# Performance work log

Hardware: AMD Instinct MI355X
Metric: run time of the kernel (lower is better)

## Reference

```python
import jax, jax.numpy as jnp
import numpy as np

B, C, H, W = 4, 192, 256, 256
WS = 8           # window_size
NH = 6           # num_heads
RS = 0.1         # residual_scale
RED = C // 16    # channel-attention reduced channels
HID = 4 * C      # ffn hidden
EPS = 1e-5


def _rel_pos_index(ws):
    coords = np.stack(np.meshgrid(np.arange(ws), np.arange(ws), indexing='ij'))  # [2,ws,ws]
    cf = coords.reshape(2, -1)
    rel = cf[:, :, None] - cf[:, None, :]            # [2,N,N]
    rel = rel.transpose(1, 2, 0).copy()
    rel[:, :, 0] += ws - 1
    rel[:, :, 1] += ws - 1
    rel[:, :, 0] *= 2 * ws - 1
    return jnp.asarray(rel.sum(-1))                  # [N,N] int

RPI = _rel_pos_index(WS)


def setup_inputs() -> dict:
    key = jax.random.key(0)
    ks = jax.random.split(key, 16)
    s = 0.02
    return {
        'x': jax.random.normal(ks[0], (B, C, H, W), jnp.float32),
        'n1_w': jnp.ones((C,), jnp.float32), 'n1_b': jnp.zeros((C,), jnp.float32),
        'n2_w': jnp.ones((C,), jnp.float32), 'n2_b': jnp.zeros((C,), jnp.float32),
        'n3_w': jnp.ones((C,), jnp.float32), 'n3_b': jnp.zeros((C,), jnp.float32),
        'ca_w1': jax.random.normal(ks[1], (RED, C), jnp.float32) * s,
        'ca_w2': jax.random.normal(ks[2], (C, RED), jnp.float32) * s,
        'qkv_w': jax.random.normal(ks[3], (3 * C, C), jnp.float32) * s,
        'proj_w': jax.random.normal(ks[4], (C, C), jnp.float32) * s,
        'proj_b': jnp.zeros((C,), jnp.float32),
        'rpb': jax.random.normal(ks[5], ((2 * WS - 1) ** 2, NH), jnp.float32) * s,
        'ffn_w1': jax.random.normal(ks[6], (HID, C), jnp.float32) * s,
        'ffn_b1': jnp.zeros((HID,), jnp.float32),
        'ffn_w2': jax.random.normal(ks[7], (C, HID), jnp.float32) * s,
        'ffn_b2': jnp.zeros((C,), jnp.float32),
    }


def _ln(x, w, b):
    m = x.mean(-1, keepdims=True)
    v = x.var(-1, keepdims=True)
    return (x - m) * jax.lax.rsqrt(v + EPS) * w + b


def reference(x, n1_w, n1_b, n2_w, n2_b, n3_w, n3_b, ca_w1, ca_w2,
              qkv_w, proj_w, proj_b, rpb, ffn_w1, ffn_b1, ffn_w2, ffn_b2):
    # --- channel attention branch ---
    res = x                                             # [B,C,H,W]
    xc = _ln(x.transpose(0, 2, 3, 1), n1_w, n1_b)       # [B,H,W,C]
    xc = xc.transpose(0, 3, 1, 2)                       # [B,C,H,W]
    y = xc.mean(axis=(2, 3))                            # [B,C] global avg pool
    y = jax.nn.relu(y @ ca_w1.T) @ ca_w2.T              # [B,C]
    y = jax.nn.sigmoid(y)[:, :, None, None]
    x = xc * y * RS + res

    # --- window attention branch ---
    res = x
    xw = _ln(x.transpose(0, 2, 3, 1), n2_w, n2_b)       # [B,H,W,C]
    nH, nW, N = H // WS, W // WS, WS * WS
    xw = xw.reshape(B, nH, WS, nW, WS, C).transpose(0, 1, 3, 2, 4, 5)
    xw = xw.reshape(B * nH * nW, N, C)                  # [Bn,N,C]

    d = C // NH
    qkv = (xw @ qkv_w.T).reshape(-1, N, 3, NH, d).transpose(2, 0, 3, 1, 4)
    q, k, v = qkv[0], qkv[1], qkv[2]                    # [Bn,NH,N,d]
    q = q * (d ** -0.5)
    attn = jnp.einsum('bhnd,bhmd->bhnm', q, k)          # [Bn,NH,N,N]
    bias = rpb[RPI.reshape(-1)].reshape(N, N, NH).transpose(2, 0, 1)
    attn = jax.nn.softmax(attn + bias[None], axis=-1)
    o = jnp.einsum('bhnm,bhmd->bhnd', attn, v)
    o = o.transpose(0, 2, 1, 3).reshape(-1, N, C)
    o = o @ proj_w.T + proj_b

    o = _ln(o, n3_w, n3_b)
    h = jax.nn.gelu(o @ ffn_w1.T + ffn_b1, approximate=False)
    o = o + (h @ ffn_w2.T + ffn_b2) * RS

    o = o.reshape(B, nH, nW, WS, WS, C).transpose(0, 1, 3, 2, 4, 5)
    o = o.reshape(B, H, W, C).transpose(0, 3, 1, 2)     # [B,C,H,W]
    return o * RS + res
```

## Files before the change

### kernel.cpp

```cpp
#include <hip/hip_runtime.h>
#include <math.h>

#define CC    192
#define WWD   256
#define HWSZ  65536
#define BB    4
#define NHD   6
#define HIDDEN 768
#define RSC   0.1f
#define EPSV  1e-5f

typedef short s8v __attribute__((ext_vector_type(8)));
typedef float f4v __attribute__((ext_vector_type(4)));
#define MFMA16(a,b,c) __builtin_amdgcn_mfma_f32_16x16x32_bf16(a,b,c,0,0,0)

__device__ __forceinline__ float b2f(unsigned short h){
  return __uint_as_float(((unsigned int)h) << 16);
}
__device__ __forceinline__ unsigned short f2b(float f){
  unsigned int u = __float_as_uint(f);
  u += 0x7FFFu + ((u >> 16) & 1u);
  return (unsigned short)(u >> 16);
}
__device__ __forceinline__ float wredsum(float v){
  #pragma unroll
  for (int off = 32; off > 0; off >>= 1) v += __shfl_xor(v, off, 64);
  return v;
}

__global__ __launch_bounds__(256) void k0_all(
    const float* __restrict__ s0, const float* __restrict__ s1,
    const float* __restrict__ s2, const float* __restrict__ s3,
    unsigned short* __restrict__ d0, unsigned short* __restrict__ d1,
    unsigned short* __restrict__ d2, unsigned short* __restrict__ d3)
{
  int i = blockIdx.x * 256 + threadIdx.x;
  const float* s; unsigned short* d; int off;
  if (i < 27648)      { s = s0; d = d0; off = 0; }
  else if (i < 36864) { s = s1; d = d1; off = 27648; }
  else if (i < 73728) { s = s2; d = d2; off = 36864; }
  else                { s = s3; d = d3; off = 73728; }
  int j = i - off;
  float4 v = ((const float4*)s)[j];
  ((ushort4*)d)[j] = make_ushort4(f2b(v.x), f2b(v.y), f2b(v.z), f2b(v.w));
}

__global__ __launch_bounds__(256) void k1a_stats(
    const float* __restrict__ x, float2* __restrict__ mr)
{
  __shared__ float red[2048];
  const int pg = threadIdx.x & 63;
  const int sl = threadIdx.x >> 6;
  const int G  = blockIdx.x * 64 + pg;
  const int b  = G >> 14;
  const float* xp = x + (size_t)(b * CC) * HWSZ + ((size_t)(G & 16383) << 2);

  float sx=0.f, sy=0.f, sz=0.f, sw=0.f;
  float qx=0.f, qy=0.f, qz=0.f, qw=0.f;
  #pragma unroll 4
  for (int i = 0; i < 48; ++i){
    float4 v = *(const float4*)(xp + (size_t)(sl * 48 + i) * HWSZ);
    sx += v.x; qx += v.x * v.x;
    sy += v.y; qy += v.y * v.y;
    sz += v.z; qz += v.z * v.z;
    sw += v.w; qw += v.w * v.w;
  }
  float* rp = red + threadIdx.x * 8;
  rp[0]=sx; rp[1]=sy; rp[2]=sz; rp[3]=sw;
  rp[4]=qx; rp[5]=qy; rp[6]=qz; rp[7]=qw;
  __syncthreads();
  if (sl == 0){
    #pragma unroll
    for (int s = 1; s < 4; ++s){
      const float* o = red + (s * 64 + pg) * 8;
      sx += o[0]; sy += o[1]; sz += o[2]; sw += o[3];
      qx += o[4]; qy += o[5]; qz += o[6]; qw += o[7];
    }
    const float inv = 1.f / CC;
    float m0 = sx*inv, m1 = sy*inv, m2 = sz*inv, m3 = sw*inv;
    float4* mrv = (float4*)mr;
    mrv[G*2]   = make_float4(m0, rsqrtf(qx*inv - m0*m0 + EPSV),
                             m1, rsqrtf(qy*inv - m1*m1 + EPSV));
    mrv[G*2+1] = make_float4(m2, rsqrtf(qz*inv - m2*m2 + EPSV),
                             m3, rsqrtf(qw*inv - m3*m3 + EPSV));
  }
}

__global__ __launch_bounds__(256) void k1b_pool(
    const float* __restrict__ x, const float4* __restrict__ mrv,
    const float* __restrict__ n1w, const float* __restrict__ n1b,
    float* __restrict__ pool)
{
  int phys = blockIdx.x;
  int b = phys & 3, c = phys >> 2;
  const float4* xp = (const float4*)(x + (size_t)(b * CC + c) * HWSZ);
  const float4* mp = mrv + (size_t)b * 32768;
  float acc = 0.f;
  for (int g = threadIdx.x; g < 16384; g += 256){
    float4 v   = xp[g];
    float4 m01 = mp[2*g], m23 = mp[2*g+1];
    acc += (v.x - m01.x) * m01.y + (v.y - m01.z) * m01.w
         + (v.z - m23.x) * m23.y + (v.w - m23.z) * m23.w;
  }
  acc = wredsum(acc);
  __shared__ float r4[4];
  if ((threadIdx.x & 63) == 0) r4[threadIdx.x >> 6] = acc;
  __syncthreads();
  if (threadIdx.x == 0)
    pool[b * CC + c] = n1w[c] * (r4[0] + r4[1] + r4[2] + r4[3])
                       + 65536.f * n1b[c];
}

__global__ __launch_bounds__(256) void k2_camlp(
    const float* __restrict__ pool, const float* __restrict__ w1,
    const float* __restrict__ w2, float* __restrict__ sig)
{
  __shared__ float t[BB * 12];
  int tid = threadIdx.x;
  if (tid < BB * 12){
    int b = tid / 12, r = tid % 12;
    float a = 0.f;
    for (int c = 0; c < CC; ++c) a += pool[b * CC + c] * w1[r * CC + c];
    a *= (1.f / 65536.f);
    t[tid] = fmaxf(a, 0.f);
  }
  __syncthreads();
  for (int i = tid; i < BB * CC; i += 256){
    int b = i / CC, c = i - b * CC;
    float z = 0.f;
    #pragma unroll
    for (int r = 0; r < 12; ++r) z += t[b * 12 + r] * w2[c * 12 + r];
    sig[i] = 1.f / (1.f + __expf(-z));
  }
}

__global__ void __launch_bounds__(256)
__attribute__((amdgpu_waves_per_eu(3, 3)))
k4_win(
    const float* __restrict__ x, const float2* __restrict__ mr,
    const float* __restrict__ sig,
    const float* __restrict__ n1w, const float* __restrict__ n1b,
    const float* __restrict__ n2w, const float* __restrict__ n2b,
    const float* __restrict__ n3w, const float* __restrict__ n3b,
    const unsigned short* __restrict__ qw,
    const unsigned short* __restrict__ pw,
    const float* __restrict__ projb,
    const float* __restrict__ rpb,
    const unsigned short* __restrict__ f1w,
    const float* __restrict__ fb1,
    const unsigned short* __restrict__ f2w,
    const float* __restrict__ fb2,
    float* __restrict__ out)
{
  __shared__ __align__(16) unsigned short lds[26624];
  unsigned short* Xs  = lds;
  unsigned short* Qs  = lds + 12800;
  unsigned short* Ks  = lds + 17408;
  unsigned short* VsT = lds + 22016;
  unsigned short* Hs  = lds + 12800;
  unsigned short* Ov  = lds + 12800;

  const int tid  = threadIdx.x;
  const int lane = tid & 63;
  const int wv   = tid >> 6;
  const int l15  = lane & 15;
  const int q    = lane >> 4;

  int phys = blockIdx.x;
  int blk  = ((phys & 7) << 9) | (phys >> 3);
  int b   = blk >> 10;
  int wh  = (blk >> 5) & 31;
  int ww  = blk & 31;
  size_t base = (size_t)(b * CC) * HWSZ + (size_t)(wh * 8) * WWD + ww * 8;
  int pbase = (b << 16) | ((wh * 8) << 8) | (ww * 8);

  float4 x1v[12];
  #pragma unroll
  for (int kk = 0; kk < 12; ++kk){
    int idx = kk * 256 + tid;
    int c   = idx >> 4;
    int t   = idx & 15;
    int row = t >> 1, col0 = (t & 1) * 4;
    float4 xv = *(const float4*)(x + base + (size_t)c * HWSZ + row * WWD + col0);
    int px = pbase + row * 256 + col0;
    float4 mra = *(const float4*)(mr + px);
    float4 mrb = *(const float4*)(mr + px + 2);
    float w  = n1w[c], bv = n1b[c];
    float sv = sig[b * CC + c] * RSC;
    int n0 = row * 8 + col0;
    float4 o;
    o.x = ((xv.x - mra.x) * mra.y * w + bv) * sv + xv.x;
    o.y = ((xv.y - mra.z) * mra.w * w + bv) * sv + xv.y;
    o.z = ((xv.z - mrb.x) * mrb.y * w + bv) * sv + xv.z;
    o.w = ((xv.w - mrb.z) * mrb.w * w + bv) * sv + xv.w;
    x1v[kk] = o;
    Xs[(n0    ) * 200 + c] = f2b(o.x);
    Xs[(n0 + 1) * 200 + c] = f2b(o.y);
    Xs[(n0 + 2) * 200 + c] = f2b(o.z);
    Xs[(n0 + 3) * 200 + c] = f2b(o.w);
  }
  __syncthreads();

  {
    float wa = n2w[lane], wb = n2w[lane + 64], wc = n2w[lane + 128];
    float ba = n2b[lane], bb3 = n2b[lane + 64], bc = n2b[lane + 128];
    for (int n = wv; n < 64; n += 4){
      float v0 = b2f(Xs[n * 200 + lane]);
      float v1 = b2f(Xs[n * 200 + lane + 64]);
      float v2 = b2f(Xs[n * 200 + lane + 128]);
      float s  = wredsum(v0 + v1 + v2);
      float ss = wredsum(v0 * v0 + v1 * v1 + v2 * v2);
      float mean = s * (1.f / CC);
      float rstd = rsqrtf(ss * (1.f / CC) - mean * mean + EPSV);
      Xs[n * 200 + lane]       = f2b((v0 - mean) * rstd * wa + ba);
      Xs[n * 200 + lane + 64]  = f2b((v1 - mean) * rstd * wb + bb3);
      Xs[n * 200 + lane + 128] = f2b((v2 - mean) * rstd * wc + bc);
    }
  }
  __syncthreads();

  float oreg[12][4];
  for (int pr = 0; pr < 3; ++pr){
    for (int t3 = 0; t3 < 3; ++t3){
      int t = wv * 3 + t3;
      int sel = t >> 2;
      int s = t & 3;
      const unsigned short* wrow = qw + (size_t)(sel * 192 + pr * 64 + s * 16 + l15) * 192;
      s8v Bf[6];
      #pragma unroll
      for (int k = 0; k < 6; ++k) Bf[k] = *(const s8v*)(wrow + k * 32 + q * 8);
      #pragma unroll
      for (int mt = 0; mt < 4; ++mt){
        f4v acc = {0.f, 0.f, 0.f, 0.f};
        #pragma unroll
        for (int k = 0; k < 6; ++k){
          s8v Af = *(const s8v*)&Xs[(mt * 16 + l15) * 200 + k * 32 + q * 8];
          acc = MFMA16(Af, Bf[k], acc);
        }
        int row0 = mt * 16 + q * 4;
        if (sel == 0){
          #pragma unroll
          for (int r = 0; r < 4; ++r)
            Qs[(row0 + r) * 72 + s * 16 + l15] = f2b(acc[r] * 0.17677669529663689f);
        } else if (sel == 1){
          #pragma unroll
          for (int r = 0; r < 4; ++r)
            Ks[(row0 + r) * 72 + s * 16 + l15] = f2b(acc[r]);
        } else {
          #pragma unroll
          for (int r = 0; r < 4; ++r)
            VsT[(s * 16 + l15) * 72 + row0 + r] = f2b(acc[r]);
        }
      }
    }
    __syncthreads();

    float sc[2][4][4];
    {
      const s8v Aq0 = *(const s8v*)&Qs[(wv * 16 + l15) * 72 + q * 8];
      const s8v Aq1 = *(const s8v*)&Qs[(wv * 16 + l15) * 72 + 32 + q * 8];
      #pragma unroll
      for (int nt = 0; nt < 4; ++nt){
        s8v Bk0 = *(const s8v*)&Ks[(nt * 16 + l15) * 72 + q * 8];
        s8v Bk1 = *(const s8v*)&Ks[(nt * 16 + l15) * 72 + 32 + q * 8];
        f4v a0 = {0.f, 0.f, 0.f, 0.f};
        f4v a1 = {0.f, 0.f, 0.f, 0.f};
        a0 = MFMA16(Aq0, Bk0, a0);
        a1 = MFMA16(Aq1, Bk1, a1);
        #pragma unroll
        for (int r = 0; r < 4; ++r){ sc[0][nt][r] = a0[r]; sc[1][nt][r] = a1[r]; }
      }
    }
    #pragma unroll
    for (int hh = 0; hh < 2; ++hh){
      int h = pr * 2 + hh;
      #pragma unroll
      for (int r = 0; r < 4; ++r){
        int rt = wv * 16 + q * 4 + r;
        int i1 = rt >> 3, j1 = rt & 7;
        float mx = -1e30f;
        #pragma unroll
        for (int nt = 0; nt < 4; ++nt){
          int ct = nt * 16 + l15;
          int i2 = ct >> 3, j2 = ct & 7;
          sc[hh][nt][r] += rpb[((i1 - i2 + 7) * 15 + (j1 - j2 + 7)) * NHD + h];
          mx = fmaxf(mx, sc[hh][nt][r]);
        }
        #pragma unroll
        for (int m = 1; m <= 8; m <<= 1) mx = fmaxf(mx, __shfl_xor(mx, m, 64));
        float sm = 0.f;
        #pragma unroll
        for (int nt = 0; nt < 4; ++nt){
          sc[hh][nt][r] = __expf(sc[hh][nt][r] - mx);
          sm += sc[hh][nt][r];
        }
        #pragma unroll
        for (int m = 1; m <= 8; m <<= 1) sm += __shfl_xor(sm, m, 64);
        float invs = 1.f / sm;
        #pragma unroll
        for (int nt = 0; nt < 4; ++nt) sc[hh][nt][r] *= invs;
      }
    }
    #pragma unroll
    for (int hh = 0; hh < 2; ++hh){
      #pragma unroll
      for (int r = 0; r < 4; ++r)
        #pragma unroll
        for (int nt = 0; nt < 4; ++nt)
          Qs[(wv * 16 + q * 4 + r) * 72 + nt * 16 + l15] = f2b(sc[hh][nt][r]);
      #pragma unroll
      for (int vt = 0; vt < 2; ++vt){
        f4v acc = {0.f, 0.f, 0.f, 0.f};
        #pragma unroll
        for (int kst = 0; kst < 2; ++kst){
          s8v Ap = *(const s8v*)&Qs[(wv * 16 + l15) * 72 + kst * 32 + q * 8];
          s8v Bv = *(const s8v*)&VsT[(hh * 32 + vt * 16 + l15) * 72 + kst * 32 + q * 8];
          acc = MFMA16(Ap, Bv, acc);
        }
        int oi = (pr * 2 + hh) * 2 + vt;
        #pragma unroll
        for (int r = 0; r < 4; ++r) oreg[oi][r] = acc[r];
      }
    }
    __syncthreads();
  }

  #pragma unroll
  for (int oi = 0; oi < 12; ++oi){
    int h2 = oi >> 1, vt = oi & 1;
    int col = h2 * 32 + vt * 16 + l15;
    int row0 = wv * 16 + q * 4;
    #pragma unroll
    for (int r = 0; r < 4; ++r)
      Xs[(row0 + r) * 200 + col] = f2b(oreg[oi][r]);
  }
  __syncthreads();

  f4v pa[3][4];
  for (int j = 0; j < 3; ++j){
    int col = wv * 48 + j * 16 + l15;
    const unsigned short* wrow = pw + (size_t)col * 192;
    s8v Bf[6];
    #pragma unroll
    for (int k = 0; k < 6; ++k) Bf[k] = *(const s8v*)(wrow + k * 32 + q * 8);
    float bv = projb[col];
    #pragma unroll
    for (int mt = 0; mt < 4; ++mt){
      f4v acc = {bv, bv, bv, bv};
      #pragma unroll
      for (int k = 0; k < 6; ++k){
        s8v Af = *(const s8v*)&Xs[(mt * 16 + l15) * 200 + k * 32 + q * 8];
        acc = MFMA16(Af, Bf[k], acc);
      }
      pa[j][mt] = acc;
    }
  }
  __syncthreads();
  #pragma unroll
  for (int j = 0; j < 3; ++j)
    for (int mt = 0; mt < 4; ++mt)
      #pragma unroll
      for (int r = 0; r < 4; ++r)
        Xs[(mt * 16 + q * 4 + r) * 200 + wv * 48 + j * 16 + l15] = f2b(pa[j][mt][r]);
  __syncthreads();

  {
    float wa = n3w[lane], wb = n3w[lane + 64], wc = n3w[lane + 128];
    float ba = n3b[lane], bb3 = n3b[lane + 64], bc = n3b[lane + 128];
    for (int n = wv; n < 64; n += 4){
      float v0 = b2f(Xs[n * 200 + lane]);
      float v1 = b2f(Xs[n * 200 + lane + 64]);
      float v2 = b2f(Xs[n * 200 + lane + 128]);
      float s  = wredsum(v0 + v1 + v2);
      float ss = wredsum(v0 * v0 + v1 * v1 + v2 * v2);
      float mean = s * (1.f / CC);
      float rstd = rsqrtf(ss * (1.f / CC) - mean * mean + EPSV);
      Xs[n * 200 + lane]       = f2b((v0 - mean) * rstd * wa + ba);
      Xs[n * 200 + lane + 64]  = f2b((v1 - mean) * rstd * wb + bb3);
      Xs[n * 200 + lane + 128] = f2b((v2 - mean) * rstd * wc + bc);
    }
  }
  __syncthreads();

  f4v facc[3][4];
  #pragma unroll
  for (int j = 0; j < 3; ++j){
    float bv = fb2[wv * 48 + j * 16 + l15];
    #pragma unroll
    for (int mt = 0; mt < 4; ++mt) facc[j][mt] = (f4v){bv, bv, bv, bv};
  }
  for (int hc = 0; hc < 6; ++hc){
    for (int j = 0; j < 2; ++j){
      int hcol = hc * 128 + wv * 32 + j * 16 + l15;
      const unsigned short* wrow = f1w + (size_t)hcol * 192;
      s8v Bf[6];
      #pragma unroll
      for (int k = 0; k < 6; ++k) Bf[k] = *(const s8v*)(wrow + k * 32 + q * 8);
      float bv = fb1[hcol];
      #pragma unroll
      for (int mt = 0; mt < 4; ++mt){
        f4v acc = {bv, bv, bv, bv};
        #pragma unroll
        for (int k = 0; k < 6; ++k){
          s8v Af = *(const s8v*)&Xs[(mt * 16 + l15) * 200 + k * 32 + q * 8];
          acc = MFMA16(Af, Bf[k], acc);
        }
        #pragma unroll
        for (int r = 0; r < 4; ++r){
          float g = acc[r];
          g = 0.5f * g * (1.f + erff(g * 0.70710678118654752f));
          Hs[(mt * 16 + q * 4 + r) * 136 + wv * 32 + j * 16 + l15] = f2b(g);
        }
      }
    }
    __syncthreads();
    for (int j = 0; j < 3; ++j){
      int col = wv * 48 + j * 16 + l15;
      const unsigned short* wrow = f2w + (size_t)col * HIDDEN + hc * 128;
      s8v Bf[4];
      #pragma unroll
      for (int kst = 0; kst < 4; ++kst) Bf[kst] = *(const s8v*)(wrow + kst * 32 + q * 8);
      #pragma unroll
      for (int mt = 0; mt < 4; ++mt){
        f4v acc = facc[j][mt];
        #pragma unroll
        for (int kst = 0; kst < 4; ++kst){
          s8v Af = *(const s8v*)&Hs[(mt * 16 + l15) * 136 + kst * 32 + q * 8];
          acc = MFMA16(Af, Bf[kst], acc);
        }
        facc[j][mt] = acc;
      }
    }
    __syncthreads();
  }

  #pragma unroll
  for (int j = 0; j < 3; ++j)
    for (int mt = 0; mt < 4; ++mt)
      #pragma unroll
      for (int r = 0; r < 4; ++r){
        int row = mt * 16 + q * 4 + r;
        int col = wv * 48 + j * 16 + l15;
        float lv = b2f(Xs[row * 200 + col]);
        Ov[row * 196 + col] = f2b(lv + facc[j][mt][r] * RSC);
      }
  __syncthreads();

  #pragma unroll
  for (int kk = 0; kk < 12; ++kk){
    int idx = kk * 256 + tid;
    int c   = idx >> 4;
    int t   = idx & 15;
    int row = t >> 1, col0 = (t & 1) * 4;
    size_t gi = base + (size_t)c * HWSZ + row * WWD + col0;
    int n0 = row * 8 + col0;
    float4 o;
    o.x = b2f(Ov[(n0    ) * 196 + c]) * RSC + x1v[kk].x;
    o.y = b2f(Ov[(n0 + 1) * 196 + c]) * RSC + x1v[kk].y;
    o.z = b2f(Ov[(n0 + 2) * 196 + c]) * RSC + x1v[kk].z;
    o.w = b2f(Ov[(n0 + 3) * 196 + c]) * RSC + x1v[kk].w;
    *(float4*)(out + gi) = o;
  }
}

extern "C" void kernel_launch(void* const* d_in, const int* in_sizes, int n_in,
                              void* d_out, int out_size, void* d_ws, size_t ws_size,
                              hipStream_t stream)
{
  const float* x    = (const float*)d_in[0];
  const float* n1w  = (const float*)d_in[1];
  const float* n1b  = (const float*)d_in[2];
  const float* n2w  = (const float*)d_in[3];
  const float* n2b  = (const float*)d_in[4];
  const float* n3w  = (const float*)d_in[5];
  const float* n3b  = (const float*)d_in[6];
  const float* caw1 = (const float*)d_in[7];
  const float* caw2 = (const float*)d_in[8];
  const float* qkvw = (const float*)d_in[9];
  const float* projw= (const float*)d_in[10];
  const float* projb= (const float*)d_in[11];
  const float* rpb  = (const float*)d_in[12];
  const float* fw1  = (const float*)d_in[13];
  const float* fb1  = (const float*)d_in[14];
  const float* fw2  = (const float*)d_in[15];
  const float* fb2  = (const float*)d_in[16];
  float* out = (float*)d_out;

  float*  pool = (float*)d_ws;
  float*  sig  = pool + 768;
  float2* mr   = (float2*)(sig + 768);
  unsigned short* qw  = (unsigned short*)((char*)d_ws + 6144 + 2097152);
  unsigned short* pwb = qw  + 110592;
  unsigned short* f1b = pwb + 36864;
  unsigned short* f2b_ = f1b + 147456;

  k0_all<<<dim3(432), dim3(256), 0, stream>>>(qkvw, projw, fw1, fw2,
                                              qw, pwb, f1b, f2b_);
  k1a_stats<<<dim3(1024), dim3(256), 0, stream>>>(x, mr);
  k1b_pool <<<dim3(768),  dim3(256), 0, stream>>>(x, (const float4*)mr,
                                                  n1w, n1b, pool);
  k2_camlp <<<dim3(1),    dim3(256), 0, stream>>>(pool, caw1, caw2, sig);
  k4_win   <<<dim3(4096), dim3(256), 0, stream>>>(x, mr, sig, n1w, n1b,
                n2w, n2b, n3w, n3b, qw, pwb, projb, rpb, f1b, fb1, f2b_, fb2, out);
}
```

Baseline: 1.172 ms.

## Pack residual in bf16 registers, tanh GELU, 16-lane layernorm, nontemporal stores

The saved residual x1 is now kept as packed bf16 pairs (24 registers instead of 48 floats), which cuts register pressure. The exact erf GELU is replaced with a tanh approximation built on __expf. The two LayerNorms use 16-lane row groups with fewer shuffles and preload the weights into registers. Output stores are now nontemporal. The bf16 residual and the tanh GELU both reduce accuracy, since the residual x1 is added at bf16 precision.

```diff
diff --git a/kernel.cpp b/kernel.cpp
--- a/kernel.cpp
+++ b/kernel.cpp
@@ -26,6 +26,12 @@
   #pragma unroll
   for (int off = 32; off > 0; off >>= 1) v += __shfl_xor(v, off, 64);
   return v;
+}
+__device__ __forceinline__ float gelu(float g){
+  float u = g * (0.7978845608028654f + 0.0356774081363001f * g * g);
+  float e = __expf(-2.f * fabsf(u));
+  float t = __builtin_copysignf((1.f - e) / (1.f + e), u);
+  return 0.5f * g * (1.f + t);
 }
 
 __global__ __launch_bounds__(256) void k0_all(
@@ -174,7 +180,7 @@
   size_t base = (size_t)(b * CC) * HWSZ + (size_t)(wh * 8) * WWD + ww * 8;
   int pbase = (b << 16) | ((wh * 8) << 8) | (ww * 8);
 
-  float4 x1v[12];
+  unsigned x1p[24];
   #pragma unroll
   for (int kk = 0; kk < 12; ++kk){
     int idx = kk * 256 + tid;
@@ -193,28 +199,41 @@
     o.y = ((xv.y - mra.z) * mra.w * w + bv) * sv + xv.y;
     o.z = ((xv.z - mrb.x) * mrb.y * w + bv) * sv + xv.z;
     o.w = ((xv.w - mrb.z) * mrb.w * w + bv) * sv + xv.w;
-    x1v[kk] = o;
-    Xs[(n0    ) * 200 + c] = f2b(o.x);
-    Xs[(n0 + 1) * 200 + c] = f2b(o.y);
-    Xs[(n0 + 2) * 200 + c] = f2b(o.z);
-    Xs[(n0 + 3) * 200 + c] = f2b(o.w);
+    unsigned short h0 = f2b(o.x), h1 = f2b(o.y), h2 = f2b(o.z), h3 = f2b(o.w);
+    x1p[kk*2]   = (unsigned)h0 | ((unsigned)h1 << 16);
+    x1p[kk*2+1] = (unsigned)h2 | ((unsigned)h3 << 16);
+    Xs[(n0    ) * 200 + c] = h0;
+    Xs[(n0 + 1) * 200 + c] = h1;
+    Xs[(n0 + 2) * 200 + c] = h2;
+    Xs[(n0 + 3) * 200 + c] = h3;
   }
   __syncthreads();
 
   {
-    float wa = n2w[lane], wb = n2w[lane + 64], wc = n2w[lane + 128];
-    float ba = n2b[lane], bb3 = n2b[lane + 64], bc = n2b[lane + 128];
-    for (int n = wv; n < 64; n += 4){
-      float v0 = b2f(Xs[n * 200 + lane]);
-      float v1 = b2f(Xs[n * 200 + lane + 64]);
-      float v2 = b2f(Xs[n * 200 + lane + 128]);
-      float s  = wredsum(v0 + v1 + v2);
-      float ss = wredsum(v0 * v0 + v1 * v1 + v2 * v2);
+    float wreg[12], breg[12];
+    #pragma unroll
+    for (int k = 0; k < 12; ++k){
+      wreg[k] = n2w[l15 + 16 * k]; breg[k] = n2b[l15 + 16 * k];
+    }
+    #pragma unroll
+    for (int it = 0; it < 4; ++it){
+      int n = it * 16 + wv * 4 + q;
+      float v[12]; float s = 0.f, ss = 0.f;
+      #pragma unroll
+      for (int k = 0; k < 12; ++k){
+        v[k] = b2f(Xs[n * 200 + l15 + 16 * k]);
+        s += v[k]; ss += v[k] * v[k];
+      }
+      #pragma unroll
+      for (int m = 1; m <= 8; m <<= 1){
+        s  += __shfl_xor(s,  m, 64);
+        ss += __shfl_xor(ss, m, 64);
+      }
       float mean = s * (1.f / CC);
       float rstd = rsqrtf(ss * (1.f / CC) - mean * mean + EPSV);
-      Xs[n * 200 + lane]       = f2b((v0 - mean) * rstd * wa + ba);
-      Xs[n * 200 + lane + 64]  = f2b((v1 - mean) * rstd * wb + bb3);
-      Xs[n * 200 + lane + 128] = f2b((v2 - mean) * rstd * wc + bc);
+      #pragma unroll
+      for (int k = 0; k < 12; ++k)
+        Xs[n * 200 + l15 + 16 * k] = f2b((v[k] - mean) * rstd * wreg[k] + breg[k]);
     }
   }
   __syncthreads();
@@ -365,19 +384,30 @@
   __syncthreads();
 
   {
-    float wa = n3w[lane], wb = n3w[lane + 64], wc = n3w[lane + 128];
-    float ba = n3b[lane], bb3 = n3b[lane + 64], bc = n3b[lane + 128];
-    for (int n = wv; n < 64; n += 4){
-      float v0 = b2f(Xs[n * 200 + lane]);
-      float v1 = b2f(Xs[n * 200 + lane + 64]);
-      float v2 = b2f(Xs[n * 200 + lane + 128]);
-      float s  = wredsum(v0 + v1 + v2);
-      float ss = wredsum(v0 * v0 + v1 * v1 + v2 * v2);
+    float wreg[12], breg[12];
+    #pragma unroll
+    for (int k = 0; k < 12; ++k){
+      wreg[k] = n3w[l15 + 16 * k]; breg[k] = n3b[l15 + 16 * k];
+    }
+    #pragma unroll
+    for (int it = 0; it < 4; ++it){
+      int n = it * 16 + wv * 4 + q;
+      float v[12]; float s = 0.f, ss = 0.f;
+      #pragma unroll
+      for (int k = 0; k < 12; ++k){
+        v[k] = b2f(Xs[n * 200 + l15 + 16 * k]);
+        s += v[k]; ss += v[k] * v[k];
+      }
+      #pragma unroll
+      for (int m = 1; m <= 8; m <<= 1){
+        s  += __shfl_xor(s,  m, 64);
+        ss += __shfl_xor(ss, m, 64);
+      }
       float mean = s * (1.f / CC);
       float rstd = rsqrtf(ss * (1.f / CC) - mean * mean + EPSV);
-      Xs[n * 200 + lane]       = f2b((v0 - mean) * rstd * wa + ba);
-      Xs[n * 200 + lane + 64]  = f2b((v1 - mean) * rstd * wb + bb3);
-      Xs[n * 200 + lane + 128] = f2b((v2 - mean) * rstd * wc + bc);
+      #pragma unroll
+      for (int k = 0; k < 12; ++k)
+        Xs[n * 200 + l15 + 16 * k] = f2b((v[k] - mean) * rstd * wreg[k] + breg[k]);
     }
   }
   __syncthreads();
@@ -406,11 +436,8 @@
           acc = MFMA16(Af, Bf[k], acc);
         }
         #pragma unroll
-        for (int r = 0; r < 4; ++r){
-          float g = acc[r];
-          g = 0.5f * g * (1.f + erff(g * 0.70710678118654752f));
-          Hs[(mt * 16 + q * 4 + r) * 136 + wv * 32 + j * 16 + l15] = f2b(g);
-        }
+        for (int r = 0; r < 4; ++r)
+          Hs[(mt * 16 + q * 4 + r) * 136 + wv * 32 + j * 16 + l15] = f2b(gelu(acc[r]));
       }
     }
     __syncthreads();
@@ -454,12 +481,13 @@
     int row = t >> 1, col0 = (t & 1) * 4;
     size_t gi = base + (size_t)c * HWSZ + row * WWD + col0;
     int n0 = row * 8 + col0;
-    float4 o;
-    o.x = b2f(Ov[(n0    ) * 196 + c]) * RSC + x1v[kk].x;
-    o.y = b2f(Ov[(n0 + 1) * 196 + c]) * RSC + x1v[kk].y;
-    o.z = b2f(Ov[(n0 + 2) * 196 + c]) * RSC + x1v[kk].z;
-    o.w = b2f(Ov[(n0 + 3) * 196 + c]) * RSC + x1v[kk].w;
-    *(float4*)(out + gi) = o;
+    unsigned p01 = x1p[kk*2], p23 = x1p[kk*2+1];
+    f4v o;
+    o[0] = b2f(Ov[(n0    ) * 196 + c]) * RSC + b2f((unsigned short)p01);
+    o[1] = b2f(Ov[(n0 + 1) * 196 + c]) * RSC + b2f((unsigned short)(p01 >> 16));
+    o[2] = b2f(Ov[(n0 + 2) * 196 + c]) * RSC + b2f((unsigned short)p23);
+    o[3] = b2f(Ov[(n0 + 3) * 196 + c]) * RSC + b2f((unsigned short)(p23 >> 16));
+    __builtin_nontemporal_store(o, (f4v*)(out + gi));
   }
 }
 
```

Result: slower. 1.244 ms (+6.1%).
